# Kernel optimization log

Measured on AMD Instinct MI355X. Metric: run time of the kernel, lower is better.

Reference implementation:

```python
import jax, jax.numpy as jnp
import numpy as np

N = 100000      # nodes
E = 1600000     # directed edges (before self loops)
IN, H, OUT = 16, 64, 8
NEG_SLOPE = 0.2  # PyG GATConv default


def setup_inputs() -> dict:
    key = jax.random.key(0)
    ks = jax.random.split(key, 12)
    g = lambda k, sh, s: (jax.random.normal(k, sh, dtype=jnp.float32) * s)
    return {
        "x": jax.random.normal(ks[0], (N, IN), dtype=jnp.float32),
        "edge_index": jax.random.randint(ks[1], (2, E), 0, N, dtype=jnp.int32),
        # layer 1 (GATConv: weight, att_src, att_dst, bias)
        "W1": g(ks[2], (IN, H), 1.0 / np.sqrt(IN)),
        "a_src1": g(ks[3], (H,), 0.1),
        "a_dst1": g(ks[4], (H,), 0.1),
        "b1": jnp.zeros((H,), jnp.float32),
        # layer 2
        "W2": g(ks[5], (H, H), 1.0 / np.sqrt(H)),
        "a_src2": g(ks[6], (H,), 0.1),
        "a_dst2": g(ks[7], (H,), 0.1),
        "b2": jnp.zeros((H,), jnp.float32),
        # policy head
        "Wp": g(ks[8], (H, OUT), 1.0 / np.sqrt(H)),
        "bp": jnp.zeros((OUT,), jnp.float32),
    }


def gat_conv(x, src, dst, W, a_src, a_dst, b):
    """PyG GATConv, heads=1: softmax over incoming edges grouped by dst."""
    h = x @ W                                   # [N, H]
    e = (h @ a_src)[src] + (h @ a_dst)[dst]      # [E'] raw attention logits
    e = jnp.where(e > 0, e, NEG_SLOPE * e)       # leaky_relu
    m = jax.ops.segment_max(e, dst, num_segments=N)
    m = jnp.where(jnp.isfinite(m), m, 0.0)       # guard empty segments
    w = jnp.exp(e - m[dst])
    den = jax.ops.segment_sum(w, dst, num_segments=N)
    alpha = w / (den[dst] + 1e-16)               # per-edge softmax weight
    out = jax.ops.segment_sum(h[src] * alpha[:, None], dst, num_segments=N)
    return out + b


def reference(x, edge_index, W1, a_src1, a_dst1, b1, W2, a_src2, a_dst2, b2, Wp, bp):
    # add self loops once (PyG default add_self_loops=True)
    loops = jnp.arange(N, dtype=edge_index.dtype)
    src = jnp.concatenate([edge_index[0], loops])
    dst = jnp.concatenate([edge_index[1], loops])
    h = jax.nn.relu(gat_conv(x, src, dst, W1, a_src1, a_dst1, b1))
    h = jax.nn.relu(gat_conv(h, src, dst, W2, a_src2, a_dst2, b2))
    return h @ Wp + bp  # [N, OUT]
```

## Files before the change

### kernel.cpp

```cpp
#include <hip/hip_runtime.h>
#include <hip/hip_fp16.h>
#include <math.h>

#define NEG_SLOPE 0.2f
#define TILE 8192

__device__ __forceinline__ float wave_reduce_sum(float v){
  #pragma unroll
  for (int off = 32; off > 0; off >>= 1) v += __shfl_xor(v, off, 64);
  return v;
}
__device__ __forceinline__ float wave_reduce_max(float v){
  #pragma unroll
  for (int off = 32; off > 0; off >>= 1) v = fmaxf(v, __shfl_xor(v, off, 64));
  return v;
}


__global__ void k_bcount(const int* __restrict__ ei, int* __restrict__ C,
                         int* __restrict__ Btot, int E, int TOT, int NB, int T){
  __shared__ int hist[512];
  int t = blockIdx.x;
  for (int i = threadIdx.x; i < NB; i += blockDim.x) hist[i] = 0;
  __syncthreads();
  int base = t * TILE;
  for (int k = threadIdx.x; k < TILE; k += blockDim.x){
    int j = base + k;
    if (j < TOT){
      int d = (j < E) ? ei[E + j] : (j - E);
      atomicAdd(&hist[d >> 8], 1);
    }
  }
  __syncthreads();
  for (int b = threadIdx.x; b < NB; b += blockDim.x){
    int v = hist[b];
    C[(size_t)b * T + t] = v;
    if (v) atomicAdd(&Btot[b], v);
  }
}

__global__ void k_bstart(const int* __restrict__ Btot, int* __restrict__ Bstart,
                         int* __restrict__ rowptr, int NB, int TOT, int N){
  __shared__ int lds[512];
  int t = threadIdx.x;
  int total = (t < NB) ? Btot[t] : 0;
  lds[t] = total; __syncthreads();
  for (int off = 1; off < 512; off <<= 1){
    int x = (t >= off) ? lds[t - off] : 0;
    __syncthreads();
    lds[t] += x;
    __syncthreads();
  }
  if (t < NB) Bstart[t] = lds[t] - total;
  if (t == 0){ Bstart[NB] = TOT; rowptr[N] = TOT; }
}

__global__ void k_bcolscan(const int* __restrict__ C, const int* __restrict__ Bstart,
                           int* __restrict__ O, int NB, int T){
  int wid = (blockIdx.x * blockDim.x + threadIdx.x) >> 6;
  int lane = threadIdx.x & 63;
  if (wid >= NB) return;
  int run = Bstart[wid];
  int nchunks = (T + 63) / 64;
  for (int i = 0; i < nchunks; i++){
    int t = i * 64 + lane;
    int v = (t < T) ? C[(size_t)wid * T + t] : 0;
    int s = v;
    #pragma unroll
    for (int off = 1; off < 64; off <<= 1){
      int u = __shfl_up(s, off);
      if (lane >= off) s += u;
    }
    if (t < T) O[(size_t)wid * T + t] = run + (s - v);
    run += __shfl(s, 63);
  }
}

__global__ void k_bscatter(const int* __restrict__ ei, const int* __restrict__ O,
                           unsigned int* __restrict__ tmp, int E, int TOT, int NB, int T){
  __shared__ int cur[512];
  int t = blockIdx.x;
  for (int b = threadIdx.x; b < NB; b += blockDim.x) cur[b] = O[(size_t)b * T + t];
  __syncthreads();
  int base = t * TILE;
  for (int k = threadIdx.x; k < TILE; k += blockDim.x){
    int j = base + k;
    if (j < TOT){
      int s, d;
      if (j < E){ s = ei[j]; d = ei[E + j]; } else { s = j - E; d = s; }
      int r = atomicAdd(&cur[d >> 8], 1);
      tmp[r] = ((unsigned)s << 8) | (unsigned)(d & 255);
    }
  }
}

__global__ void k_bfinal(const unsigned int* __restrict__ tmp, const int* __restrict__ Bstart,
                         int* __restrict__ rowptr, int* __restrict__ col, int N){
  __shared__ int hist[256];
  __shared__ int sc[256];
  __shared__ int cur[256];
  int b = blockIdx.x;
  int base_node = b << 8;
  int nnode = min(256, N - base_node);
  int beg = Bstart[b], end = Bstart[b + 1];
  int t = threadIdx.x;
  hist[t] = 0;
  __syncthreads();
  for (int j = beg + t; j < end; j += blockDim.x)
    atomicAdd(&hist[tmp[j] & 255u], 1);
  __syncthreads();
  int v = hist[t];
  sc[t] = v; __syncthreads();
  for (int off = 1; off < 256; off <<= 1){
    int x = (t >= off) ? sc[t - off] : 0;
    __syncthreads();
    sc[t] += x;
    __syncthreads();
  }
  int excl = sc[t] - v;
  if (t < nnode) rowptr[base_node + t] = beg + excl;
  cur[t] = beg + excl;
  __syncthreads();
  for (int j = beg + t; j < end; j += blockDim.x){
    unsigned u = tmp[j];
    int pos = atomicAdd(&cur[u & 255u], 1);
    col[pos] = (int)(u >> 8);
  }
}


__global__ void k_dense16(const float* __restrict__ x, const float* __restrict__ W,
                          const float* __restrict__ asrc, const float* __restrict__ adst,
                          __half* __restrict__ h16, float* __restrict__ sarr, float* __restrict__ darr,
                          int n){
  __shared__ float4 Ws4[16 * 16];
  __shared__ float as_s[64], ad_s[64];
  int t = threadIdx.x;
  const float4* W4 = (const float4*)W;
  if (t < 16 * 16) Ws4[t] = W4[t];
  if (t < 64){ as_s[t] = asrc[t]; ad_s[t] = adst[t]; }
  __syncthreads();
  int gid = blockIdx.x * blockDim.x + t;
  int node = gid >> 1;
  int half = gid & 1;
  if (node >= n) return;
  const float4* xr = (const float4*)(x + (size_t)node * 16);
  float4 acc[8] = {};
  #pragma unroll
  for (int kk = 0; kk < 4; kk++){
    float4 xv = xr[kk];
    #pragma unroll
    for (int i = 0; i < 4; i++){
      float xk = (i == 0) ? xv.x : (i == 1) ? xv.y : (i == 2) ? xv.z : xv.w;
      const float4* wrow = &Ws4[(kk * 4 + i) * 16 + half * 8];
      #pragma unroll
      for (int c = 0; c < 8; c++){
        acc[c].x = fmaf(xk, wrow[c].x, acc[c].x);
        acc[c].y = fmaf(xk, wrow[c].y, acc[c].y);
        acc[c].z = fmaf(xk, wrow[c].z, acc[c].z);
        acc[c].w = fmaf(xk, wrow[c].w, acc[c].w);
      }
    }
  }
  float sv = 0.f, dv = 0.f;
  #pragma unroll
  for (int c = 0; c < 8; c += 2){
    union { __half2 h2[4]; uint4 u; } pk;
    pk.h2[0] = __floats2half2_rn(acc[c].x,   acc[c].y);
    pk.h2[1] = __floats2half2_rn(acc[c].z,   acc[c].w);
    pk.h2[2] = __floats2half2_rn(acc[c+1].x, acc[c+1].y);
    pk.h2[3] = __floats2half2_rn(acc[c+1].z, acc[c+1].w);
    *(uint4*)(h16 + (size_t)node * 64 + half * 32 + c * 4) = pk.u;
  }
  #pragma unroll
  for (int c = 0; c < 8; c++){
    int cb = half * 32 + c * 4;
    sv += acc[c].x * as_s[cb] + acc[c].y * as_s[cb+1] + acc[c].z * as_s[cb+2] + acc[c].w * as_s[cb+3];
    dv += acc[c].x * ad_s[cb] + acc[c].y * ad_s[cb+1] + acc[c].z * ad_s[cb+2] + acc[c].w * ad_s[cb+3];
  }
  sv += __shfl_xor(sv, 1);
  dv += __shfl_xor(dv, 1);
  if (half == 0){ sarr[node] = sv; darr[node] = dv; }
}

__global__ void k_dense64(const float* __restrict__ x, const float* __restrict__ W,
                          const float* __restrict__ asrc, const float* __restrict__ adst,
                          __half* __restrict__ h16, float* __restrict__ sarr, float* __restrict__ darr,
                          int n){
  __shared__ float4 Ws4[64 * 16];
  __shared__ float as_s[64], ad_s[64];
  int t = threadIdx.x;
  const float4* W4 = (const float4*)W;
  for (int i = t; i < 64 * 16; i += blockDim.x) Ws4[i] = W4[i];
  if (t < 64){ as_s[t] = asrc[t]; ad_s[t] = adst[t]; }
  __syncthreads();
  int gid = blockIdx.x * blockDim.x + t;
  int node = gid >> 1;
  int half = gid & 1;
  if (node >= n) return;
  const float4* xr = (const float4*)(x + (size_t)node * 64);
  float4 acc[8] = {};
  #pragma unroll
  for (int kk = 0; kk < 16; kk++){
    float4 xv = xr[kk];
    #pragma unroll
    for (int i = 0; i < 4; i++){
      float xk = (i == 0) ? xv.x : (i == 1) ? xv.y : (i == 2) ? xv.z : xv.w;
      const float4* wrow = &Ws4[(kk * 4 + i) * 16 + half * 8];
      #pragma unroll
      for (int c = 0; c < 8; c++){
        acc[c].x = fmaf(xk, wrow[c].x, acc[c].x);
        acc[c].y = fmaf(xk, wrow[c].y, acc[c].y);
        acc[c].z = fmaf(xk, wrow[c].z, acc[c].z);
        acc[c].w = fmaf(xk, wrow[c].w, acc[c].w);
      }
    }
  }
  float sv = 0.f, dv = 0.f;
  #pragma unroll
  for (int c = 0; c < 8; c += 2){
    union { __half2 h2[4]; uint4 u; } pk;
    pk.h2[0] = __floats2half2_rn(acc[c].x,   acc[c].y);
    pk.h2[1] = __floats2half2_rn(acc[c].z,   acc[c].w);
    pk.h2[2] = __floats2half2_rn(acc[c+1].x, acc[c+1].y);
    pk.h2[3] = __floats2half2_rn(acc[c+1].z, acc[c+1].w);
    *(uint4*)(h16 + (size_t)node * 64 + half * 32 + c * 4) = pk.u;
  }
  #pragma unroll
  for (int c = 0; c < 8; c++){
    int cb = half * 32 + c * 4;
    sv += acc[c].x * as_s[cb] + acc[c].y * as_s[cb+1] + acc[c].z * as_s[cb+2] + acc[c].w * as_s[cb+3];
    dv += acc[c].x * ad_s[cb] + acc[c].y * ad_s[cb+1] + acc[c].z * ad_s[cb+2] + acc[c].w * ad_s[cb+3];
  }
  sv += __shfl_xor(sv, 1);
  dv += __shfl_xor(dv, 1);
  if (half == 0){ sarr[node] = sv; darr[node] = dv; }
}


__device__ __forceinline__ void agg_softmax(const float* sarr, const int* col,
                                            int beg, int deg, float dn, int lane,
                                            int& c0, int& c1, float& a0, float& a1){
  c0 = 0; c1 = 0;
  float e0 = -INFINITY, e1 = -INFINITY;
  if (lane < deg){
    c0 = col[beg + lane];
    float t = sarr[c0] + dn;
    e0 = (t > 0.f) ? t : NEG_SLOPE * t;
  }
  if (lane + 64 < deg){
    c1 = col[beg + lane + 64];
    float t = sarr[c1] + dn;
    e1 = (t > 0.f) ? t : NEG_SLOPE * t;
  }
  float m = wave_reduce_max(fmaxf(e0, e1));
  float w0 = (lane < deg)      ? __expf(e0 - m) : 0.f;
  float w1 = (lane + 64 < deg) ? __expf(e1 - m) : 0.f;
  float sum = wave_reduce_sum(w0 + w1);
  float inv = 1.f / (sum + 1e-16f);
  a0 = w0 * inv; a1 = w1 * inv;
}

__device__ __forceinline__ void agg_gather16(const __half* h16, int deg, int lane,
                                             const int2* stash, float4& A0, float4& A1){
  int eg = lane & 7, co = lane >> 3;
  float4 a0v = make_float4(0.f,0.f,0.f,0.f), a1v = make_float4(0.f,0.f,0.f,0.f);
  #pragma unroll 2
  for (int j0 = 0; j0 < deg; j0 += 8){
    int idx = j0 + eg;
    if (idx < deg){
      int2 ca = stash[idx];
      float a = __int_as_float(ca.y);
      uint4 raw = *(const uint4*)(h16 + (size_t)ca.x * 64 + co * 8);
      float2 f0 = __half22float2(*(__half2*)&raw.x);
      float2 f1 = __half22float2(*(__half2*)&raw.y);
      float2 f2 = __half22float2(*(__half2*)&raw.z);
      float2 f3 = __half22float2(*(__half2*)&raw.w);
      a0v.x = fmaf(a, f0.x, a0v.x); a0v.y = fmaf(a, f0.y, a0v.y);
      a0v.z = fmaf(a, f1.x, a0v.z); a0v.w = fmaf(a, f1.y, a0v.w);
      a1v.x = fmaf(a, f2.x, a1v.x); a1v.y = fmaf(a, f2.y, a1v.y);
      a1v.z = fmaf(a, f3.x, a1v.z); a1v.w = fmaf(a, f3.y, a1v.w);
    }
  }
  #pragma unroll
  for (int off = 1; off < 8; off <<= 1){
    a0v.x += __shfl_xor(a0v.x, off); a0v.y += __shfl_xor(a0v.y, off);
    a0v.z += __shfl_xor(a0v.z, off); a0v.w += __shfl_xor(a0v.w, off);
    a1v.x += __shfl_xor(a1v.x, off); a1v.y += __shfl_xor(a1v.y, off);
    a1v.z += __shfl_xor(a1v.z, off); a1v.w += __shfl_xor(a1v.w, off);
  }
  A0 = a0v; A1 = a1v;
}

__global__ void k_agg1(const __half* __restrict__ h16, const float* __restrict__ sarr,
                       const float* __restrict__ darr, const int* __restrict__ rowptr,
                       const int* __restrict__ col, const float* __restrict__ bias,
                       float* __restrict__ out, int n){
  __shared__ int2 stash[4][128];
  int w = threadIdx.x >> 6;
  int lane = threadIdx.x & 63;
  int node = blockIdx.x * (blockDim.x >> 6) + w;
  if (node >= n) return;
  int beg = rowptr[node];
  int deg = rowptr[node + 1] - beg;
  float dn = darr[node];

  if (deg <= 128){
    int c0, c1; float a0, a1;
    agg_softmax(sarr, col, beg, deg, dn, lane, c0, c1, a0, a1);
    if (lane < deg)      stash[w][lane]      = make_int2(c0, __float_as_int(a0));
    if (lane + 64 < deg) stash[w][lane + 64] = make_int2(c1, __float_as_int(a1));
    float4 A0, A1;
    agg_gather16(h16, deg, lane, stash[w], A0, A1);
    int eg = lane & 7, co = lane >> 3;
    if (eg == 0){
      const float4 b0 = *(const float4*)(bias + co * 8);
      const float4 b1 = *(const float4*)(bias + co * 8 + 4);
      float4 r0, r1;
      r0.x = fmaxf(A0.x + b0.x, 0.f); r0.y = fmaxf(A0.y + b0.y, 0.f);
      r0.z = fmaxf(A0.z + b0.z, 0.f); r0.w = fmaxf(A0.w + b0.w, 0.f);
      r1.x = fmaxf(A1.x + b1.x, 0.f); r1.y = fmaxf(A1.y + b1.y, 0.f);
      r1.z = fmaxf(A1.z + b1.z, 0.f); r1.w = fmaxf(A1.w + b1.w, 0.f);
      *(float4*)(out + (size_t)node * 64 + co * 8)     = r0;
      *(float4*)(out + (size_t)node * 64 + co * 8 + 4) = r1;
    }
  } else {
    float m = -INFINITY;
    int end = beg + deg;
    for (int j = beg + lane; j < end; j += 64){
      float e = sarr[col[j]] + dn;
      e = (e > 0.f) ? e : NEG_SLOPE * e;
      m = fmaxf(m, e);
    }
    m = wave_reduce_max(m);
    float sum = 0.f;
    for (int j = beg + lane; j < end; j += 64){
      float e = sarr[col[j]] + dn;
      e = (e > 0.f) ? e : NEG_SLOPE * e;
      sum += __expf(e - m);
    }
    sum = wave_reduce_sum(sum);
    float invden = 1.0f / (sum + 1e-16f);
    float acc = 0.f;
    for (int j = beg; j < end; j++){
      int s = col[j];
      float e = sarr[s] + dn;
      e = (e > 0.f) ? e : NEG_SLOPE * e;
      float alpha = __expf(e - m) * invden;
      acc = fmaf(alpha, __half2float(h16[(size_t)s * 64 + lane]), acc);
    }
    float r = acc + bias[lane];
    out[(size_t)node * 64 + lane] = fmaxf(r, 0.f);
  }
}

__global__ void k_agg2(const __half* __restrict__ h16, const float* __restrict__ sarr,
                       const float* __restrict__ darr, const int* __restrict__ rowptr,
                       const int* __restrict__ col, const float* __restrict__ bias,
                       const float* __restrict__ Wp, const float* __restrict__ bp,
                       float* __restrict__ out, int n){
  __shared__ int2 stash[4][128];
  int w = threadIdx.x >> 6;
  int lane = threadIdx.x & 63;
  int o = lane & 7, g = lane >> 3;
  float wp[8];
  #pragma unroll
  for (int j = 0; j < 8; j++) wp[j] = Wp[(g * 8 + j) * 8 + o];
  float bpv = bp[o];

  int node = blockIdx.x * (blockDim.x >> 6) + w;
  if (node >= n) return;
  int beg = rowptr[node];
  int deg = rowptr[node + 1] - beg;
  float dn = darr[node];

  if (deg <= 128){
    int c0, c1; float a0, a1;
    agg_softmax(sarr, col, beg, deg, dn, lane, c0, c1, a0, a1);
    if (lane < deg)      stash[w][lane]      = make_int2(c0, __float_as_int(a0));
    if (lane + 64 < deg) stash[w][lane + 64] = make_int2(c1, __float_as_int(a1));
    float4 A0, A1;
    agg_gather16(h16, deg, lane, stash[w], A0, A1);
    const float4 b0 = *(const float4*)(bias + g * 8);
    const float4 b1 = *(const float4*)(bias + g * 8 + 4);
    float r0 = fmaxf(A0.x + b0.x, 0.f), r1 = fmaxf(A0.y + b0.y, 0.f);
    float r2 = fmaxf(A0.z + b0.z, 0.f), r3 = fmaxf(A0.w + b0.w, 0.f);
    float r4 = fmaxf(A1.x + b1.x, 0.f), r5 = fmaxf(A1.y + b1.y, 0.f);
    float r6 = fmaxf(A1.z + b1.z, 0.f), r7 = fmaxf(A1.w + b1.w, 0.f);
    float po = r0*wp[0] + r1*wp[1] + r2*wp[2] + r3*wp[3]
             + r4*wp[4] + r5*wp[5] + r6*wp[6] + r7*wp[7];
    po += __shfl_xor(po, 8);
    po += __shfl_xor(po, 16);
    po += __shfl_xor(po, 32);
    if (lane < 8) out[(size_t)node * 8 + lane] = po + bpv;
  } else {
    int end = beg + deg;
    float m = -INFINITY;
    for (int j = beg + lane; j < end; j += 64){
      float e = sarr[col[j]] + dn;
      e = (e > 0.f) ? e : NEG_SLOPE * e;
      m = fmaxf(m, e);
    }
    m = wave_reduce_max(m);
    float sum = 0.f;
    for (int j = beg + lane; j < end; j += 64){
      float e = sarr[col[j]] + dn;
      e = (e > 0.f) ? e : NEG_SLOPE * e;
      sum += __expf(e - m);
    }
    sum = wave_reduce_sum(sum);
    float invden = 1.0f / (sum + 1e-16f);
    float acc = 0.f;
    for (int j = beg; j < end; j++){
      int s = col[j];
      float e = sarr[s] + dn;
      e = (e > 0.f) ? e : NEG_SLOPE * e;
      float alpha = __expf(e - m) * invden;
      acc = fmaf(alpha, __half2float(h16[(size_t)s * 64 + lane]), acc);
    }
    float r = fmaxf(acc + bias[lane], 0.f);
    float po = 0.f;
    #pragma unroll
    for (int j = 0; j < 8; j++) po += __shfl(r, g * 8 + j) * wp[j];
    po += __shfl_xor(po, 8);
    po += __shfl_xor(po, 16);
    po += __shfl_xor(po, 32);
    if (lane < 8) out[(size_t)node * 8 + lane] = po + bpv;
  }
}


extern "C" void kernel_launch(void* const* d_in, const int* in_sizes, int n_in,
                              void* d_out, int out_size, void* d_ws, size_t ws_size,
                              hipStream_t stream) {
  const float* x   = (const float*)d_in[0];
  const int*   ei  = (const int*)  d_in[1];
  const float* W1  = (const float*)d_in[2];
  const float* as1 = (const float*)d_in[3];
  const float* ad1 = (const float*)d_in[4];
  const float* b1  = (const float*)d_in[5];
  const float* W2  = (const float*)d_in[6];
  const float* as2 = (const float*)d_in[7];
  const float* ad2 = (const float*)d_in[8];
  const float* b2  = (const float*)d_in[9];
  const float* Wp  = (const float*)d_in[10];
  const float* bp  = (const float*)d_in[11];
  float* out = (float*)d_out;

  int N = in_sizes[0] / 16;
  int E = in_sizes[1] / 2;
  int TOT = E + N;
  int NB = (N + 255) >> 8;
  int T  = (TOT + TILE - 1) / TILE;

  char* p = (char*)d_ws;
  auto alloc = [&](size_t bytes) -> char* {
    char* r = p; p += (bytes + 255) & ~(size_t)255; return r;
  };
  __half* h16   = (__half*)alloc((size_t)N * 64 * 2);
  float* buf    = (float*)alloc((size_t)N * 64 * 4);
  float* sA     = (float*)alloc((size_t)N * 4);
  float* dA     = (float*)alloc((size_t)N * 4);
  int*   rowptr = (int*)  alloc((size_t)(N + 1) * 4);
  int*   col    = (int*)  alloc((size_t)TOT * 4);
  int*   Bstart = (int*)  alloc((size_t)(NB + 1) * 4);
  int*   Btot   = (int*)  alloc((size_t)(NB + 1) * 4);

  unsigned int* tmp  = (unsigned int*)h16;
  int*          Cmat = (int*)buf;
  int*          Omat = Cmat + (size_t)NB * T;

  const int tb = 256;

  (void)hipMemsetAsync(Btot, 0, (size_t)(NB + 1) * 4, stream);
  k_bcount<<<T, tb, 0, stream>>>(ei, Cmat, Btot, E, TOT, NB, T);
  k_bstart<<<1, 512, 0, stream>>>(Btot, Bstart, rowptr, NB, TOT, N);
  k_bcolscan<<<(NB + 3) / 4, tb, 0, stream>>>(Cmat, Bstart, Omat, NB, T);
  k_bscatter<<<T, tb, 0, stream>>>(ei, Omat, tmp, E, TOT, NB, T);
  k_bfinal<<<NB, tb, 0, stream>>>(tmp, Bstart, rowptr, col, N);

  k_dense16<<<(2 * N + tb - 1) / tb, tb, 0, stream>>>(x, W1, as1, ad1, h16, sA, dA, N);
  k_agg1<<<(N + 3) / 4, 256, 0, stream>>>(h16, sA, dA, rowptr, col, b1, buf, N);
  k_dense64<<<(2 * N + tb - 1) / tb, tb, 0, stream>>>(buf, W2, as2, ad2, h16, sA, dA, N);
  k_agg2<<<(N + 3) / 4, 256, 0, stream>>>(h16, sA, dA, rowptr, col, b2, Wp, bp, out, N);
}
```

Measured before the change: 222.4 us.

## Process two destination nodes per wavefront in GAT aggregation kernels

Each wavefront now handles two destination nodes instead of one, running both softmax passes and then a fused dual gather that interleaves loads for both nodes' neighbor rows. The aim is more memory-level parallelism per wave and less per-node fixed overhead, since average degree is about 17 and leaves most of the 8-edge-group gather loop underused. In exchange the grid is halved, register pressure rises, and the loop runs to the larger of the two degrees, which adds divergence.

```diff
diff --git a/kernel.cpp b/kernel.cpp
--- a/kernel.cpp
+++ b/kernel.cpp
@@ -292,65 +292,178 @@
   A0 = a0v; A1 = a1v;
 }
 
+__device__ __forceinline__ void agg_gather16x2(const __half* h16, int degA, int degB,
+                                               int lane, const int2* stA, const int2* stB,
+                                               float4& A0, float4& A1, float4& B0, float4& B1){
+  int eg = lane & 7, co = lane >> 3;
+  float4 a0v = make_float4(0.f,0.f,0.f,0.f), a1v = make_float4(0.f,0.f,0.f,0.f);
+  float4 b0v = make_float4(0.f,0.f,0.f,0.f), b1v = make_float4(0.f,0.f,0.f,0.f);
+  int maxd = max(degA, degB);
+  #pragma unroll 2
+  for (int j0 = 0; j0 < maxd; j0 += 8){
+    int idx = j0 + eg;
+    bool okA = idx < degA, okB = idx < degB;
+    int2 ca = make_int2(0, 0), cb = make_int2(0, 0);
+    if (okA) ca = stA[idx];
+    if (okB) cb = stB[idx];
+    uint4 rawA = make_uint4(0,0,0,0), rawB = make_uint4(0,0,0,0);
+    if (okA) rawA = *(const uint4*)(h16 + (size_t)ca.x * 64 + co * 8);
+    if (okB) rawB = *(const uint4*)(h16 + (size_t)cb.x * 64 + co * 8);
+    if (okA){
+      float a = __int_as_float(ca.y);
+      float2 f0 = __half22float2(*(__half2*)&rawA.x);
+      float2 f1 = __half22float2(*(__half2*)&rawA.y);
+      float2 f2 = __half22float2(*(__half2*)&rawA.z);
+      float2 f3 = __half22float2(*(__half2*)&rawA.w);
+      a0v.x = fmaf(a, f0.x, a0v.x); a0v.y = fmaf(a, f0.y, a0v.y);
+      a0v.z = fmaf(a, f1.x, a0v.z); a0v.w = fmaf(a, f1.y, a0v.w);
+      a1v.x = fmaf(a, f2.x, a1v.x); a1v.y = fmaf(a, f2.y, a1v.y);
+      a1v.z = fmaf(a, f3.x, a1v.z); a1v.w = fmaf(a, f3.y, a1v.w);
+    }
+    if (okB){
+      float a = __int_as_float(cb.y);
+      float2 f0 = __half22float2(*(__half2*)&rawB.x);
+      float2 f1 = __half22float2(*(__half2*)&rawB.y);
+      float2 f2 = __half22float2(*(__half2*)&rawB.z);
+      float2 f3 = __half22float2(*(__half2*)&rawB.w);
+      b0v.x = fmaf(a, f0.x, b0v.x); b0v.y = fmaf(a, f0.y, b0v.y);
+      b0v.z = fmaf(a, f1.x, b0v.z); b0v.w = fmaf(a, f1.y, b0v.w);
+      b1v.x = fmaf(a, f2.x, b1v.x); b1v.y = fmaf(a, f2.y, b1v.y);
+      b1v.z = fmaf(a, f3.x, b1v.z); b1v.w = fmaf(a, f3.y, b1v.w);
+    }
+  }
+  #pragma unroll
+  for (int off = 1; off < 8; off <<= 1){
+    a0v.x += __shfl_xor(a0v.x, off); a0v.y += __shfl_xor(a0v.y, off);
+    a0v.z += __shfl_xor(a0v.z, off); a0v.w += __shfl_xor(a0v.w, off);
+    a1v.x += __shfl_xor(a1v.x, off); a1v.y += __shfl_xor(a1v.y, off);
+    a1v.z += __shfl_xor(a1v.z, off); a1v.w += __shfl_xor(a1v.w, off);
+    b0v.x += __shfl_xor(b0v.x, off); b0v.y += __shfl_xor(b0v.y, off);
+    b0v.z += __shfl_xor(b0v.z, off); b0v.w += __shfl_xor(b0v.w, off);
+    b1v.x += __shfl_xor(b1v.x, off); b1v.y += __shfl_xor(b1v.y, off);
+    b1v.z += __shfl_xor(b1v.z, off); b1v.w += __shfl_xor(b1v.w, off);
+  }
+  A0 = a0v; A1 = a1v; B0 = b0v; B1 = b1v;
+}
+
+__device__ __forceinline__ float agg_slow(const __half* h16, const float* sarr,
+                                          const int* col, int beg, int deg, float dn, int lane){
+  int end = beg + deg;
+  float m = -INFINITY;
+  for (int j = beg + lane; j < end; j += 64){
+    float e = sarr[col[j]] + dn;
+    e = (e > 0.f) ? e : NEG_SLOPE * e;
+    m = fmaxf(m, e);
+  }
+  m = wave_reduce_max(m);
+  float sum = 0.f;
+  for (int j = beg + lane; j < end; j += 64){
+    float e = sarr[col[j]] + dn;
+    e = (e > 0.f) ? e : NEG_SLOPE * e;
+    sum += __expf(e - m);
+  }
+  sum = wave_reduce_sum(sum);
+  float invden = 1.0f / (sum + 1e-16f);
+  float acc = 0.f;
+  for (int j = beg; j < end; j++){
+    int s = col[j];
+    float e = sarr[s] + dn;
+    e = (e > 0.f) ? e : NEG_SLOPE * e;
+    float alpha = __expf(e - m) * invden;
+    acc = fmaf(alpha, __half2float(h16[(size_t)s * 64 + lane]), acc);
+  }
+  return acc;
+}
+
 __global__ void k_agg1(const __half* __restrict__ h16, const float* __restrict__ sarr,
                        const float* __restrict__ darr, const int* __restrict__ rowptr,
                        const int* __restrict__ col, const float* __restrict__ bias,
                        float* __restrict__ out, int n){
-  __shared__ int2 stash[4][128];
+  __shared__ int2 stash[4][2][128];
   int w = threadIdx.x >> 6;
   int lane = threadIdx.x & 63;
-  int node = blockIdx.x * (blockDim.x >> 6) + w;
-  if (node >= n) return;
-  int beg = rowptr[node];
-  int deg = rowptr[node + 1] - beg;
-  float dn = darr[node];
-
-  if (deg <= 128){
+  int eg = lane & 7, co = lane >> 3;
+  int nodeA = blockIdx.x * 8 + w * 2;
+  int nodeB = nodeA + 1;
+  if (nodeA >= n) return;
+  bool vB = nodeB < n;
+
+  int begA = rowptr[nodeA], degA = rowptr[nodeA + 1] - begA;
+  float dnA = darr[nodeA];
+  int begB = 0, degB = 0; float dnB = 0.f;
+  if (vB){ begB = rowptr[nodeB]; degB = rowptr[nodeB + 1] - begB; dnB = darr[nodeB]; }
+  bool fastA = degA <= 128;
+  bool fastB = vB && degB <= 128;
+
+  if (fastA){
     int c0, c1; float a0, a1;
-    agg_softmax(sarr, col, beg, deg, dn, lane, c0, c1, a0, a1);
-    if (lane < deg)      stash[w][lane]      = make_int2(c0, __float_as_int(a0));
-    if (lane + 64 < deg) stash[w][lane + 64] = make_int2(c1, __float_as_int(a1));
-    float4 A0, A1;
-    agg_gather16(h16, deg, lane, stash[w], A0, A1);
-    int eg = lane & 7, co = lane >> 3;
+    agg_softmax(sarr, col, begA, degA, dnA, lane, c0, c1, a0, a1);
+    if (lane < degA)      stash[w][0][lane]      = make_int2(c0, __float_as_int(a0));
+    if (lane + 64 < degA) stash[w][0][lane + 64] = make_int2(c1, __float_as_int(a1));
+  }
+  if (fastB){
+    int c0, c1; float a0, a1;
+    agg_softmax(sarr, col, begB, degB, dnB, lane, c0, c1, a0, a1);
+    if (lane < degB)      stash[w][1][lane]      = make_int2(c0, __float_as_int(a0));
+    if (lane + 64 < degB) stash[w][1][lane + 64] = make_int2(c1, __float_as_int(a1));
+  }
+
+  const float4 b0 = *(const float4*)(bias + co * 8);
+  const float4 b1 = *(const float4*)(bias + co * 8 + 4);
+
+  if (fastA && fastB){
+    float4 A0, A1, B0, B1;
+    agg_gather16x2(h16, degA, degB, lane, stash[w][0], stash[w][1], A0, A1, B0, B1);
     if (eg == 0){
-      const float4 b0 = *(const float4*)(bias + co * 8);
-      const float4 b1 = *(const float4*)(bias + co * 8 + 4);
       float4 r0, r1;
       r0.x = fmaxf(A0.x + b0.x, 0.f); r0.y = fmaxf(A0.y + b0.y, 0.f);
       r0.z = fmaxf(A0.z + b0.z, 0.f); r0.w = fmaxf(A0.w + b0.w, 0.f);
       r1.x = fmaxf(A1.x + b1.x, 0.f); r1.y = fmaxf(A1.y + b1.y, 0.f);
       r1.z = fmaxf(A1.z + b1.z, 0.f); r1.w = fmaxf(A1.w + b1.w, 0.f);
-      *(float4*)(out + (size_t)node * 64 + co * 8)     = r0;
-      *(float4*)(out + (size_t)node * 64 + co * 8 + 4) = r1;
+      *(float4*)(out + (size_t)nodeA * 64 + co * 8)     = r0;
+      *(float4*)(out + (size_t)nodeA * 64 + co * 8 + 4) = r1;
+      r0.x = fmaxf(B0.x + b0.x, 0.f); r0.y = fmaxf(B0.y + b0.y, 0.f);
+      r0.z = fmaxf(B0.z + b0.z, 0.f); r0.w = fmaxf(B0.w + b0.w, 0.f);
+      r1.x = fmaxf(B1.x + b1.x, 0.f); r1.y = fmaxf(B1.y + b1.y, 0.f);
+      r1.z = fmaxf(B1.z + b1.z, 0.f); r1.w = fmaxf(B1.w + b1.w, 0.f);
+      *(float4*)(out + (size_t)nodeB * 64 + co * 8)     = r0;
+      *(float4*)(out + (size_t)nodeB * 64 + co * 8 + 4) = r1;
     }
   } else {
-    float m = -INFINITY;
-    int end = beg + deg;
-    for (int j = beg + lane; j < end; j += 64){
-      float e = sarr[col[j]] + dn;
-      e = (e > 0.f) ? e : NEG_SLOPE * e;
-      m = fmaxf(m, e);
-    }
-    m = wave_reduce_max(m);
-    float sum = 0.f;
-    for (int j = beg + lane; j < end; j += 64){
-      float e = sarr[col[j]] + dn;
-      e = (e > 0.f) ? e : NEG_SLOPE * e;
-      sum += __expf(e - m);
-    }
-    sum = wave_reduce_sum(sum);
-    float invden = 1.0f / (sum + 1e-16f);
-    float acc = 0.f;
-    for (int j = beg; j < end; j++){
-      int s = col[j];
-      float e = sarr[s] + dn;
-      e = (e > 0.f) ? e : NEG_SLOPE * e;
-      float alpha = __expf(e - m) * invden;
-      acc = fmaf(alpha, __half2float(h16[(size_t)s * 64 + lane]), acc);
-    }
-    float r = acc + bias[lane];
-    out[(size_t)node * 64 + lane] = fmaxf(r, 0.f);
+    if (fastA){
+      float4 A0, A1;
+      agg_gather16(h16, degA, lane, stash[w][0], A0, A1);
+      if (eg == 0){
+        float4 r0, r1;
+        r0.x = fmaxf(A0.x + b0.x, 0.f); r0.y = fmaxf(A0.y + b0.y, 0.f);
+        r0.z = fmaxf(A0.z + b0.z, 0.f); r0.w = fmaxf(A0.w + b0.w, 0.f);
+        r1.x = fmaxf(A1.x + b1.x, 0.f); r1.y = fmaxf(A1.y + b1.y, 0.f);
+        r1.z = fmaxf(A1.z + b1.z, 0.f); r1.w = fmaxf(A1.w + b1.w, 0.f);
+        *(float4*)(out + (size_t)nodeA * 64 + co * 8)     = r0;
+        *(float4*)(out + (size_t)nodeA * 64 + co * 8 + 4) = r1;
+      }
+    } else {
+      float acc = agg_slow(h16, sarr, col, begA, degA, dnA, lane);
+      out[(size_t)nodeA * 64 + lane] = fmaxf(acc + bias[lane], 0.f);
+    }
+    if (vB){
+      if (fastB){
+        float4 A0, A1;
+        agg_gather16(h16, degB, lane, stash[w][1], A0, A1);
+        if (eg == 0){
+          float4 r0, r1;
+          r0.x = fmaxf(A0.x + b0.x, 0.f); r0.y = fmaxf(A0.y + b0.y, 0.f);
+          r0.z = fmaxf(A0.z + b0.z, 0.f); r0.w = fmaxf(A0.w + b0.w, 0.f);
+          r1.x = fmaxf(A1.x + b1.x, 0.f); r1.y = fmaxf(A1.y + b1.y, 0.f);
+          r1.z = fmaxf(A1.z + b1.z, 0.f); r1.w = fmaxf(A1.w + b1.w, 0.f);
+          *(float4*)(out + (size_t)nodeB * 64 + co * 8)     = r0;
+          *(float4*)(out + (size_t)nodeB * 64 + co * 8 + 4) = r1;
+        }
+      } else {
+        float acc = agg_slow(h16, sarr, col, begB, degB, dnB, lane);
+        out[(size_t)nodeB * 64 + lane] = fmaxf(acc + bias[lane], 0.f);
+      }
+    }
   }
 }
 
@@ -359,7 +472,7 @@
                        const int* __restrict__ col, const float* __restrict__ bias,
                        const float* __restrict__ Wp, const float* __restrict__ bp,
                        float* __restrict__ out, int n){
-  __shared__ int2 stash[4][128];
+  __shared__ int2 stash[4][2][128];
   int w = threadIdx.x >> 6;
   int lane = threadIdx.x & 63;
   int o = lane & 7, g = lane >> 3;
@@ -368,64 +481,99 @@
   for (int j = 0; j < 8; j++) wp[j] = Wp[(g * 8 + j) * 8 + o];
   float bpv = bp[o];
 
-  int node = blockIdx.x * (blockDim.x >> 6) + w;
-  if (node >= n) return;
-  int beg = rowptr[node];
-  int deg = rowptr[node + 1] - beg;
-  float dn = darr[node];
-
-  if (deg <= 128){
+  int nodeA = blockIdx.x * 8 + w * 2;
+  int nodeB = nodeA + 1;
+  if (nodeA >= n) return;
+  bool vB = nodeB < n;
+
+  int begA = rowptr[nodeA], degA = rowptr[nodeA + 1] - begA;
+  float dnA = darr[nodeA];
+  int begB = 0, degB = 0; float dnB = 0.f;
+  if (vB){ begB = rowptr[nodeB]; degB = rowptr[nodeB + 1] - begB; dnB = darr[nodeB]; }
+  bool fastA = degA <= 128;
+  bool fastB = vB && degB <= 128;
+
+  if (fastA){
     int c0, c1; float a0, a1;
-    agg_softmax(sarr, col, beg, deg, dn, lane, c0, c1, a0, a1);
-    if (lane < deg)      stash[w][lane]      = make_int2(c0, __float_as_int(a0));
-    if (lane + 64 < deg) stash[w][lane + 64] = make_int2(c1, __float_as_int(a1));
-    float4 A0, A1;
-    agg_gather16(h16, deg, lane, stash[w], A0, A1);
-    const float4 b0 = *(const float4*)(bias + g * 8);
-    const float4 b1 = *(const float4*)(bias + g * 8 + 4);
+    agg_softmax(sarr, col, begA, degA, dnA, lane, c0, c1, a0, a1);
+    if (lane < degA)      stash[w][0][lane]      = make_int2(c0, __float_as_int(a0));
+    if (lane + 64 < degA) stash[w][0][lane + 64] = make_int2(c1, __float_as_int(a1));
+  }
+  if (fastB){
+    int c0, c1; float a0, a1;
+    agg_softmax(sarr, col, begB, degB, dnB, lane, c0, c1, a0, a1);
+    if (lane < degB)      stash[w][1][lane]      = make_int2(c0, __float_as_int(a0));
+    if (lane + 64 < degB) stash[w][1][lane + 64] = make_int2(c1, __float_as_int(a1));
+  }
+
+  const float4 b0 = *(const float4*)(bias + g * 8);
+  const float4 b1 = *(const float4*)(bias + g * 8 + 4);
+
+  if (fastA && fastB){
+    float4 A0, A1, B0, B1;
+    agg_gather16x2(h16, degA, degB, lane, stash[w][0], stash[w][1], A0, A1, B0, B1);
     float r0 = fmaxf(A0.x + b0.x, 0.f), r1 = fmaxf(A0.y + b0.y, 0.f);
     float r2 = fmaxf(A0.z + b0.z, 0.f), r3 = fmaxf(A0.w + b0.w, 0.f);
     float r4 = fmaxf(A1.x + b1.x, 0.f), r5 = fmaxf(A1.y + b1.y, 0.f);
     float r6 = fmaxf(A1.z + b1.z, 0.f), r7 = fmaxf(A1.w + b1.w, 0.f);
-    float po = r0*wp[0] + r1*wp[1] + r2*wp[2] + r3*wp[3]
-             + r4*wp[4] + r5*wp[5] + r6*wp[6] + r7*wp[7];
-    po += __shfl_xor(po, 8);
-    po += __shfl_xor(po, 16);
-    po += __shfl_xor(po, 32);
-    if (lane < 8) out[(size_t)node * 8 + lane] = po + bpv;
+    float poA = r0*wp[0] + r1*wp[1] + r2*wp[2] + r3*wp[3]
+              + r4*wp[4] + r5*wp[5] + r6*wp[6] + r7*wp[7];
+    r0 = fmaxf(B0.x + b0.x, 0.f); r1 = fmaxf(B0.y + b0.y, 0.f);
+    r2 = fmaxf(B0.z + b0.z, 0.f); r3 = fmaxf(B0.w + b0.w, 0.f);
+    r4 = fmaxf(B1.x + b1.x, 0.f); r5 = fmaxf(B1.y + b1.y, 0.f);
+    r6 = fmaxf(B1.z + b1.z, 0.f); r7 = fmaxf(B1.w + b1.w, 0.f);
+    float poB = r0*wp[0] + r1*wp[1] + r2*wp[2] + r3*wp[3]
+              + r4*wp[4] + r5*wp[5] + r6*wp[6] + r7*wp[7];
+    poA += __shfl_xor(poA, 8);  poB += __shfl_xor(poB, 8);
+    poA += __shfl_xor(poA, 16); poB += __shfl_xor(poB, 16);
+    poA += __shfl_xor(poA, 32); poB += __shfl_xor(poB, 32);
+    if (lane < 8){
+      out[(size_t)nodeA * 8 + lane] = poA + bpv;
+      out[(size_t)nodeB * 8 + lane] = poB + bpv;
+    }
   } else {
-    int end = beg + deg;
-    float m = -INFINITY;
-    for (int j = beg + lane; j < end; j += 64){
-      float e = sarr[col[j]] + dn;
-      e = (e > 0.f) ? e : NEG_SLOPE * e;
-      m = fmaxf(m, e);
-    }
-    m = wave_reduce_max(m);
-    float sum = 0.f;
-    for (int j = beg + lane; j < end; j += 64){
-      float e = sarr[col[j]] + dn;
-      e = (e > 0.f) ? e : NEG_SLOPE * e;
-      sum += __expf(e - m);
-    }
-    sum = wave_reduce_sum(sum);
-    float invden = 1.0f / (sum + 1e-16f);
-    float acc = 0.f;
-    for (int j = beg; j < end; j++){
-      int s = col[j];
-      float e = sarr[s] + dn;
-      e = (e > 0.f) ? e : NEG_SLOPE * e;
-      float alpha = __expf(e - m) * invden;
-      acc = fmaf(alpha, __half2float(h16[(size_t)s * 64 + lane]), acc);
-    }
-    float r = fmaxf(acc + bias[lane], 0.f);
-    float po = 0.f;
-    #pragma unroll
-    for (int j = 0; j < 8; j++) po += __shfl(r, g * 8 + j) * wp[j];
-    po += __shfl_xor(po, 8);
-    po += __shfl_xor(po, 16);
-    po += __shfl_xor(po, 32);
-    if (lane < 8) out[(size_t)node * 8 + lane] = po + bpv;
+    if (fastA){
+      float4 A0, A1;
+      agg_gather16(h16, degA, lane, stash[w][0], A0, A1);
+      float r0 = fmaxf(A0.x + b0.x, 0.f), r1 = fmaxf(A0.y + b0.y, 0.f);
+      float r2 = fmaxf(A0.z + b0.z, 0.f), r3 = fmaxf(A0.w + b0.w, 0.f);
+      float r4 = fmaxf(A1.x + b1.x, 0.f), r5 = fmaxf(A1.y + b1.y, 0.f);
+      float r6 = fmaxf(A1.z + b1.z, 0.f), r7 = fmaxf(A1.w + b1.w, 0.f);
+      float po = r0*wp[0] + r1*wp[1] + r2*wp[2] + r3*wp[3]
+               + r4*wp[4] + r5*wp[5] + r6*wp[6] + r7*wp[7];
+      po += __shfl_xor(po, 8); po += __shfl_xor(po, 16); po += __shfl_xor(po, 32);
+      if (lane < 8) out[(size_t)nodeA * 8 + lane] = po + bpv;
+    } else {
+      float acc = agg_slow(h16, sarr, col, begA, degA, dnA, lane);
+      float r = fmaxf(acc + bias[lane], 0.f);
+      float po = 0.f;
+      #pragma unroll
+      for (int j = 0; j < 8; j++) po += __shfl(r, g * 8 + j) * wp[j];
+      po += __shfl_xor(po, 8); po += __shfl_xor(po, 16); po += __shfl_xor(po, 32);
+      if (lane < 8) out[(size_t)nodeA * 8 + lane] = po + bpv;
+    }
+    if (vB){
+      if (fastB){
+        float4 A0, A1;
+        agg_gather16(h16, degB, lane, stash[w][1], A0, A1);
+        float r0 = fmaxf(A0.x + b0.x, 0.f), r1 = fmaxf(A0.y + b0.y, 0.f);
+        float r2 = fmaxf(A0.z + b0.z, 0.f), r3 = fmaxf(A0.w + b0.w, 0.f);
+        float r4 = fmaxf(A1.x + b1.x, 0.f), r5 = fmaxf(A1.y + b1.y, 0.f);
+        float r6 = fmaxf(A1.z + b1.z, 0.f), r7 = fmaxf(A1.w + b1.w, 0.f);
+        float po = r0*wp[0] + r1*wp[1] + r2*wp[2] + r3*wp[3]
+                 + r4*wp[4] + r5*wp[5] + r6*wp[6] + r7*wp[7];
+        po += __shfl_xor(po, 8); po += __shfl_xor(po, 16); po += __shfl_xor(po, 32);
+        if (lane < 8) out[(size_t)nodeB * 8 + lane] = po + bpv;
+      } else {
+        float acc = agg_slow(h16, sarr, col, begB, degB, dnB, lane);
+        float r = fmaxf(acc + bias[lane], 0.f);
+        float po = 0.f;
+        #pragma unroll
+        for (int j = 0; j < 8; j++) po += __shfl(r, g * 8 + j) * wp[j];
+        po += __shfl_xor(po, 8); po += __shfl_xor(po, 16); po += __shfl_xor(po, 32);
+        if (lane < 8) out[(size_t)nodeB * 8 + lane] = po + bpv;
+      }
+    }
   }
 }
 
@@ -480,7 +628,7 @@
   k_bfinal<<<NB, tb, 0, stream>>>(tmp, Bstart, rowptr, col, N);
 
   k_dense16<<<(2 * N + tb - 1) / tb, tb, 0, stream>>>(x, W1, as1, ad1, h16, sA, dA, N);
-  k_agg1<<<(N + 3) / 4, 256, 0, stream>>>(h16, sA, dA, rowptr, col, b1, buf, N);
+  k_agg1<<<(N + 7) / 8, 256, 0, stream>>>(h16, sA, dA, rowptr, col, b1, buf, N);
   k_dense64<<<(2 * N + tb - 1) / tb, tb, 0, stream>>>(buf, W2, as2, ad2, h16, sA, dA, N);
-  k_agg2<<<(N + 3) / 4, 256, 0, stream>>>(h16, sA, dA, rowptr, col, b2, Wp, bp, out, N);
-}
+  k_agg2<<<(N + 7) / 8, 256, 0, stream>>>(h16, sA, dA, rowptr, col, b2, Wp, bp, out, N);
+}
```

New measurement: 215.0 us. 1.03x faster.
